# Performance work log

Measured on AMD Instinct MI355X. Metric: run time of the kernel, lower is better.

## Reference

```python
import jax, jax.numpy as jnp
import numpy as np

N, D = 16384, 2048


def setup_inputs() -> dict:
    key = jax.random.key(0)
    k1, k2, k3, k4 = jax.random.split(key, 4)
    X = jax.random.normal(k1, (N, D), dtype=jnp.float32)
    keep = jax.random.uniform(k4, (N, D)) > 0.5
    X = jnp.where(keep, X, 0.0)
    A = jax.random.normal(k2, (D, D), dtype=jnp.float32)
    b = jax.random.normal(k3, (D,), dtype=jnp.float32)
    return {"X": X, "A": A, "b": b}


def reference(X, A, b):
    # y_pred = X @ A.T + b
    y_pred = jnp.einsum('nd,kd->nk', X, A) + b  # [N, D]
    mask = X != 0
    masked = jnp.where(mask, y_pred, 0.0)
    row_sum = masked.sum(axis=1, keepdims=True)          # [N, 1]
    has_any = mask.any(axis=1, keepdims=True)            # [N, 1]
    y_out = jnp.where(mask, masked / row_sum, 0.0)
    # rows with an empty mask stay all-zero (matches the Python-loop guard)
    y_out = jnp.where(has_any, y_out, 0.0)
    return y_out
```

## Files before the change

### kernel.cpp

```cpp
#include <hip/hip_runtime.h>

#define N_ROWS 16384
#define D_DIM  2048
#define BM 128
#define BN 128
#define BK 32
#define NKT (D_DIM / BK)

typedef __attribute__((ext_vector_type(8)))  _Float16 half8;
typedef __attribute__((ext_vector_type(4)))  _Float16 half4_t;
typedef __attribute__((ext_vector_type(4)))  float floatx4;

typedef __attribute__((address_space(1))) const unsigned int as1_uint;
typedef __attribute__((address_space(3))) unsigned int as3_uint;

__device__ __forceinline__ void gload_lds16(const _Float16* g, _Float16* l) {
    __builtin_amdgcn_global_load_lds((as1_uint*)g, (as3_uint*)l, 16, 0, 0);
}

__global__ void split_all_kernel(const float4* __restrict__ Xs,
                                 half4_t* __restrict__ Xdh,
                                 half4_t* __restrict__ Xdl,
                                 unsigned char* __restrict__ mask,
                                 const float4* __restrict__ As,
                                 half4_t* __restrict__ Adh,
                                 half4_t* __restrict__ Adl,
                                 int nX8, int total8)
{
    int i = blockIdx.x * blockDim.x + threadIdx.x;
    if (i >= total8) return;

    const float4* src; half4_t* dh; half4_t* dl; int j; bool domask;
    if (i < nX8) { src = Xs; dh = Xdh; dl = Xdl; j = i;       domask = true;  }
    else         { src = As; dh = Adh; dl = Adl; j = i - nX8; domask = false; }

    float4 a = src[2 * j];
    float4 b = src[2 * j + 1];
    half4_t ha, la, hb, lb;
    ha[0] = (_Float16)a.x; ha[1] = (_Float16)a.y;
    ha[2] = (_Float16)a.z; ha[3] = (_Float16)a.w;
    la[0] = (_Float16)((a.x - (float)ha[0]) * 4096.0f);
    la[1] = (_Float16)((a.y - (float)ha[1]) * 4096.0f);
    la[2] = (_Float16)((a.z - (float)ha[2]) * 4096.0f);
    la[3] = (_Float16)((a.w - (float)ha[3]) * 4096.0f);
    hb[0] = (_Float16)b.x; hb[1] = (_Float16)b.y;
    hb[2] = (_Float16)b.z; hb[3] = (_Float16)b.w;
    lb[0] = (_Float16)((b.x - (float)hb[0]) * 4096.0f);
    lb[1] = (_Float16)((b.y - (float)hb[1]) * 4096.0f);
    lb[2] = (_Float16)((b.z - (float)hb[2]) * 4096.0f);
    lb[3] = (_Float16)((b.w - (float)hb[3]) * 4096.0f);
    dh[2 * j] = ha; dh[2 * j + 1] = hb;
    dl[2 * j] = la; dl[2 * j + 1] = lb;
    if (domask) {
        unsigned int m = 0;
        m |= (a.x != 0.0f) ? 0x01u : 0u;  m |= (a.y != 0.0f) ? 0x02u : 0u;
        m |= (a.z != 0.0f) ? 0x04u : 0u;  m |= (a.w != 0.0f) ? 0x08u : 0u;
        m |= (b.x != 0.0f) ? 0x10u : 0u;  m |= (b.y != 0.0f) ? 0x20u : 0u;
        m |= (b.z != 0.0f) ? 0x40u : 0u;  m |= (b.w != 0.0f) ? 0x80u : 0u;
        mask[j] = (unsigned char)m;
    }
}

__global__ __launch_bounds__(256, 2)
void gemm_presplit_kernel(const _Float16* __restrict__ Xh,
                          const _Float16* __restrict__ Xl,
                          const _Float16* __restrict__ Ah,
                          const _Float16* __restrict__ Al,
                          const unsigned char* __restrict__ maskbits,
                          const float* __restrict__ bias,
                          float* __restrict__ out,
                          float* __restrict__ partials)
{
    __shared__ __align__(16) _Float16 sXh[2][BM * BK];
    __shared__ __align__(16) _Float16 sXl[2][BM * BK];
    __shared__ __align__(16) _Float16 sAh[2][BN * BK];
    __shared__ __align__(16) _Float16 sAl[2][BN * BK];

    const int t   = threadIdx.x;
    const int bid = blockIdx.x;

    const int xcd    = bid & 7;
    const int local  = bid >> 3;
    const int r_tile = (xcd << 4) + (local & 15);
    const int c_tile = local >> 4;
    const int m0 = r_tile * BM;
    const int n0 = c_tile * BN;

    const int lane  = t & 63;
    const int w     = t >> 6;
    const int wr    = w >> 1;
    const int wc    = w & 1;
    const int lrow  = lane & 15;
    const int lslot = lane >> 4;

    floatx4 acc1[4][4], acc2[4][4];
    #pragma unroll
    for (int mi = 0; mi < 4; ++mi)
        #pragma unroll
        for (int ni = 0; ni < 4; ++ni)
            #pragma unroll
            for (int j = 0; j < 4; ++j) { acc1[mi][ni][j] = 0.f; acc2[mi][ni][j] = 0.f; }

    const _Float16* gsrc;
    _Float16* lb0; _Float16* lb1;
    if      (w == 0) { gsrc = Xh + (size_t)m0 * D_DIM; lb0 = &sXh[0][0]; lb1 = &sXh[1][0]; }
    else if (w == 1) { gsrc = Xl + (size_t)m0 * D_DIM; lb0 = &sXl[0][0]; lb1 = &sXl[1][0]; }
    else if (w == 2) { gsrc = Ah + (size_t)n0 * D_DIM; lb0 = &sAh[0][0]; lb1 = &sAh[1][0]; }
    else             { gsrc = Al + (size_t)n0 * D_DIM; lb0 = &sAl[0][0]; lb1 = &sAl[1][0]; }

    int off8[8];
    #pragma unroll
    for (int i = 0; i < 8; ++i) {
        int c = i * 64 + lane;
        int row = c >> 2;
        int sp  = c & 3;
        int kslot = sp ^ ((row >> 1) & 3);
        off8[i] = row * D_DIM + kslot * 8;
    }

    auto issue = [&](int buf, int kt) {
        _Float16* lb = buf ? lb1 : lb0;
        const _Float16* gk = gsrc + kt * BK;
        #pragma unroll
        for (int i = 0; i < 8; ++i)
            gload_lds16(gk + off8[i], lb + i * 512);
    };

    issue(0, 0);

    int cur = 0;
    for (int kt = 0; kt < NKT; ++kt) {
        __syncthreads();
        if (kt + 1 < NKT) issue(cur ^ 1, kt + 1);

        half8 bhf[4], blf[4];
        #pragma unroll
        for (int ni = 0; ni < 4; ++ni) {
            int row = wc * 64 + ni * 16 + lrow;
            int off = row * BK + ((lslot ^ ((row >> 1) & 3)) << 3);
            bhf[ni] = *reinterpret_cast<const half8*>(&sAh[cur][off]);
            blf[ni] = *reinterpret_cast<const half8*>(&sAl[cur][off]);
        }
        #pragma unroll
        for (int mi = 0; mi < 4; ++mi) {
            int row = wr * 64 + mi * 16 + lrow;
            int off = row * BK + ((lslot ^ ((row >> 1) & 3)) << 3);
            half8 ah = *reinterpret_cast<const half8*>(&sXh[cur][off]);
            half8 al = *reinterpret_cast<const half8*>(&sXl[cur][off]);
            #pragma unroll
            for (int ni = 0; ni < 4; ++ni) {
                acc1[mi][ni] = __builtin_amdgcn_mfma_f32_16x16x32_f16(ah, bhf[ni], acc1[mi][ni], 0, 0, 0);
                acc2[mi][ni] = __builtin_amdgcn_mfma_f32_16x16x32_f16(ah, blf[ni], acc2[mi][ni], 0, 0, 0);
                acc2[mi][ni] = __builtin_amdgcn_mfma_f32_16x16x32_f16(al, bhf[ni], acc2[mi][ni], 0, 0, 0);
            }
        }
        cur ^= 1;
    }

    #pragma unroll
    for (int mi = 0; mi < 4; ++mi) {
        float rs[4];
        #pragma unroll
        for (int j = 0; j < 4; ++j) rs[j] = 0.f;
        #pragma unroll
        for (int ni = 0; ni < 4; ++ni) {
            int c = n0 + wc * 64 + ni * 16 + lrow;
            float bv = bias[c];
            #pragma unroll
            for (int j = 0; j < 4; ++j) {
                int r = m0 + wr * 64 + mi * 16 + lslot * 4 + j;
                size_t idx = (size_t)r * D_DIM + c;
                float v = acc1[mi][ni][j] + acc2[mi][ni][j] * (1.0f / 4096.0f) + bv;
                unsigned int bit = (maskbits[idx >> 3] >> (c & 7)) & 1u;
                float mv = bit ? v : 0.0f;
                out[idx] = mv;
                rs[j] += mv;
            }
        }
        #pragma unroll
        for (int j = 0; j < 4; ++j) {
            float s = rs[j];
            s += __shfl_xor(s, 1, 64);
            s += __shfl_xor(s, 2, 64);
            s += __shfl_xor(s, 4, 64);
            s += __shfl_xor(s, 8, 64);
            if (lrow == 0) {
                int r = m0 + wr * 64 + mi * 16 + lslot * 4 + j;
                partials[(size_t)r * 32 + c_tile * 2 + wc] = s;
            }
        }
    }
}

__global__ void partial_inv_kernel(const float4* __restrict__ p4, float* __restrict__ inv)
{
    int gid  = blockIdx.x * 256 + threadIdx.x;
    int r    = gid >> 3;
    int slot = gid & 7;
    float4 v = p4[(size_t)r * 8 + slot];
    float s = (v.x + v.y) + (v.z + v.w);
    s += __shfl_xor(s, 1, 64);
    s += __shfl_xor(s, 2, 64);
    s += __shfl_xor(s, 4, 64);
    if (slot == 0) inv[r] = (s != 0.0f) ? (1.0f / s) : 0.0f;
}

__global__ __launch_bounds__(256, 2)
void gemm_mask_kernel(const float* __restrict__ X,
                      const float* __restrict__ A,
                      const float* __restrict__ bias,
                      float* __restrict__ out)
{
    __shared__ __align__(16) _Float16 sXh[2][BM * BK];
    __shared__ __align__(16) _Float16 sXl[2][BM * BK];
    __shared__ __align__(16) _Float16 sAh[2][BN * BK];
    __shared__ __align__(16) _Float16 sAl[2][BN * BK];

    const int t   = threadIdx.x;
    const int bid = blockIdx.x;
    const int xcd    = bid & 7;
    const int local  = bid >> 3;
    const int r_tile = (xcd << 4) + (local & 15);
    const int c_tile = local >> 4;
    const int m0 = r_tile * BM;
    const int n0 = c_tile * BN;

    const int lane  = t & 63;
    const int w     = t >> 6;
    const int wr    = w >> 1;
    const int wc    = w & 1;
    const int lrow  = lane & 15;
    const int lslot = lane >> 4;

    const float4* X4 = reinterpret_cast<const float4*>(X);
    const float4* A4 = reinterpret_cast<const float4*>(A);

    floatx4 acc1[4][4], acc2[4][4];
    #pragma unroll
    for (int mi = 0; mi < 4; ++mi)
        #pragma unroll
        for (int ni = 0; ni < 4; ++ni)
            #pragma unroll
            for (int j = 0; j < 4; ++j) { acc1[mi][ni][j] = 0.f; acc2[mi][ni][j] = 0.f; }

    float4 rx[4], ra[4];
    #pragma unroll
    for (int i = 0; i < 4; ++i) {
        int f = i * 256 + t; int row = f >> 3; int k4 = f & 7;
        rx[i] = X4[(size_t)(m0 + row) * (D_DIM / 4) + k4];
        ra[i] = A4[(size_t)(n0 + row) * (D_DIM / 4) + k4];
    }

    auto stage = [&](const float4* rv, _Float16* dsh, _Float16* dsl) {
        #pragma unroll
        for (int i = 0; i < 4; ++i) {
            int f = i * 256 + t; int row = f >> 3; int k4 = f & 7;
            float4 v = rv[i];
            half4_t h, l;
            h[0] = (_Float16)v.x; h[1] = (_Float16)v.y;
            h[2] = (_Float16)v.z; h[3] = (_Float16)v.w;
            l[0] = (_Float16)((v.x - (float)h[0]) * 4096.0f);
            l[1] = (_Float16)((v.y - (float)h[1]) * 4096.0f);
            l[2] = (_Float16)((v.z - (float)h[2]) * 4096.0f);
            l[3] = (_Float16)((v.w - (float)h[3]) * 4096.0f);
            int off = row * BK + ((((k4 >> 1) ^ ((row >> 1) & 3)) << 3) + ((k4 & 1) << 2));
            *reinterpret_cast<half4_t*>(dsh + off) = h;
            *reinterpret_cast<half4_t*>(dsl + off) = l;
        }
    };

    stage(rx, &sXh[0][0], &sXl[0][0]);
    stage(ra, &sAh[0][0], &sAl[0][0]);

    int cur = 0;
    for (int kt = 0; kt < NKT; ++kt) {
        __syncthreads();
        const bool more = (kt + 1 < NKT);
        if (more) {
            int kb = (kt + 1) * (BK / 4);
            #pragma unroll
            for (int i = 0; i < 4; ++i) {
                int f = i * 256 + t; int row = f >> 3; int k4 = f & 7;
                rx[i] = X4[(size_t)(m0 + row) * (D_DIM / 4) + kb + k4];
                ra[i] = A4[(size_t)(n0 + row) * (D_DIM / 4) + kb + k4];
            }
        }

        half8 bhf[4], blf[4];
        #pragma unroll
        for (int ni = 0; ni < 4; ++ni) {
            int row = wc * 64 + ni * 16 + lrow;
            int off = row * BK + ((lslot ^ ((row >> 1) & 3)) << 3);
            bhf[ni] = *reinterpret_cast<const half8*>(&sAh[cur][off]);
            blf[ni] = *reinterpret_cast<const half8*>(&sAl[cur][off]);
        }
        #pragma unroll
        for (int mi = 0; mi < 4; ++mi) {
            int row = wr * 64 + mi * 16 + lrow;
            int off = row * BK + ((lslot ^ ((row >> 1) & 3)) << 3);
            half8 ah = *reinterpret_cast<const half8*>(&sXh[cur][off]);
            half8 al = *reinterpret_cast<const half8*>(&sXl[cur][off]);
            #pragma unroll
            for (int ni = 0; ni < 4; ++ni) {
                acc1[mi][ni] = __builtin_amdgcn_mfma_f32_16x16x32_f16(ah, bhf[ni], acc1[mi][ni], 0, 0, 0);
                acc2[mi][ni] = __builtin_amdgcn_mfma_f32_16x16x32_f16(ah, blf[ni], acc2[mi][ni], 0, 0, 0);
                acc2[mi][ni] = __builtin_amdgcn_mfma_f32_16x16x32_f16(al, bhf[ni], acc2[mi][ni], 0, 0, 0);
            }
        }

        if (more) {
            int nxt = cur ^ 1;
            stage(rx, &sXh[nxt][0], &sXl[nxt][0]);
            stage(ra, &sAh[nxt][0], &sAl[nxt][0]);
            cur = nxt;
        }
    }

    #pragma unroll
    for (int mi = 0; mi < 4; ++mi) {
        #pragma unroll
        for (int ni = 0; ni < 4; ++ni) {
            int c = n0 + wc * 64 + ni * 16 + lrow;
            float bv = bias[c];
            #pragma unroll
            for (int j = 0; j < 4; ++j) {
                int r = m0 + wr * 64 + mi * 16 + lslot * 4 + j;
                float v = acc1[mi][ni][j] + acc2[mi][ni][j] * (1.0f / 4096.0f) + bv;
                float xv = X[(size_t)r * D_DIM + c];
                out[(size_t)r * D_DIM + c] = (xv != 0.0f) ? v : 0.0f;
            }
        }
    }
}

__global__ void row_sum_inv_kernel(const float* __restrict__ out, float* __restrict__ inv)
{
    int gw = (blockIdx.x * 256 + threadIdx.x) >> 6;
    int l  = threadIdx.x & 63;
    const float4* row = reinterpret_cast<const float4*>(out) + (size_t)gw * (D_DIM / 4);
    float s = 0.f;
    #pragma unroll
    for (int j = 0; j < 8; ++j) {
        float4 v = row[j * 64 + l];
        s += (v.x + v.y) + (v.z + v.w);
    }
    #pragma unroll
    for (int off = 32; off > 0; off >>= 1) s += __shfl_down(s, off, 64);
    if (l == 0) inv[gw] = (s != 0.0f) ? (1.0f / s) : 0.0f;
}

__global__ void scale_kernel(float* __restrict__ out, const float* __restrict__ inv)
{
    const int total = N_ROWS * (D_DIM / 4);
    float4* o = reinterpret_cast<float4*>(out);
    for (int i = blockIdx.x * blockDim.x + threadIdx.x; i < total;
         i += gridDim.x * blockDim.x) {
        float s  = inv[i >> 9];
        float4 v = o[i];
        v.x *= s; v.y *= s; v.z *= s; v.w *= s;
        o[i] = v;
    }
}

extern "C" void kernel_launch(void* const* d_in, const int* in_sizes, int n_in,
                              void* d_out, int out_size, void* d_ws, size_t ws_size,
                              hipStream_t stream)
{
    const float* X  = (const float*)d_in[0];
    const float* A  = (const float*)d_in[1];
    const float* b  = (const float*)d_in[2];
    float* out = (float*)d_out;

    const size_t nX = (size_t)N_ROWS * D_DIM;
    const size_t nA = (size_t)D_DIM * D_DIM;
    const size_t inv_bytes  = (size_t)N_ROWS * sizeof(float);
    const size_t part_bytes = (size_t)N_ROWS * 32 * sizeof(float);
    const size_t mask_bytes = nX / 8;
    const size_t need = inv_bytes + part_bytes + 2 * nX * 2 + 2 * nA * 2 + mask_bytes;

    if (ws_size >= need) {
        float*         inv  = (float*)d_ws;
        float*         part = (float*)((char*)d_ws + inv_bytes);
        _Float16*      Xh   = (_Float16*)((char*)d_ws + inv_bytes + part_bytes);
        _Float16*      Xl   = Xh + nX;
        _Float16*      Ah   = Xl + nX;
        _Float16*      Al   = Ah + nA;
        unsigned char* mb   = (unsigned char*)(Al + nA);

        const int nX8    = (int)(nX / 8);
        const int total8 = (int)((nX + nA) / 8);
        hipLaunchKernelGGL(split_all_kernel, dim3((total8 + 255) / 256), dim3(256), 0, stream,
                           (const float4*)X, (half4_t*)Xh, (half4_t*)Xl, mb,
                           (const float4*)A, (half4_t*)Ah, (half4_t*)Al,
                           nX8, total8);
        hipLaunchKernelGGL(gemm_presplit_kernel, dim3((N_ROWS / BM) * (D_DIM / BN)), dim3(256), 0, stream,
                           Xh, Xl, Ah, Al, mb, b, out, part);
        hipLaunchKernelGGL(partial_inv_kernel, dim3(N_ROWS * 8 / 256), dim3(256), 0, stream,
                           (const float4*)part, inv);
        hipLaunchKernelGGL(scale_kernel, dim3(2048), dim3(256), 0, stream, out, inv);
    } else {
        float* inv = (float*)d_ws;
        hipLaunchKernelGGL(gemm_mask_kernel, dim3((N_ROWS / BM) * (D_DIM / BN)), dim3(256), 0, stream,
                           X, A, b, out);
        hipLaunchKernelGGL(row_sum_inv_kernel, dim3(N_ROWS / 4), dim3(256), 0, stream, out, inv);
        hipLaunchKernelGGL(scale_kernel, dim3(2048), dim3(256), 0, stream, out, inv);
    }
}
```

Measured before the change: 479.0 us.

## Load A fragments directly from global and fuse row-sum inverse into scaling

The GEMM kernel stops staging the A operand (high and low halves) through LDS. Each wave now reads its B fragments straight from global memory every k-step, and all four waves share the X-tile async loads. This halves LDS usage and may allow higher occupancy, but it adds uncoalesced global or L2 reads of A with no software prefetch. Separately, the partial-sum-to-inverse kernel is merged into the scale kernel, saving one launch and the inv buffer round trip.

After: 714.1 us. 49.1% more time.

```diff
diff --git a/kernel.cpp b/kernel.cpp
--- a/kernel.cpp
+++ b/kernel.cpp
@@ -73,8 +73,6 @@
 {
     __shared__ __align__(16) _Float16 sXh[2][BM * BK];
     __shared__ __align__(16) _Float16 sXl[2][BM * BK];
-    __shared__ __align__(16) _Float16 sAh[2][BN * BK];
-    __shared__ __align__(16) _Float16 sAl[2][BN * BK];
 
     const int t   = threadIdx.x;
     const int bid = blockIdx.x;
@@ -101,32 +99,37 @@
             #pragma unroll
             for (int j = 0; j < 4; ++j) { acc1[mi][ni][j] = 0.f; acc2[mi][ni][j] = 0.f; }
 
-    const _Float16* gsrc;
-    _Float16* lb0; _Float16* lb1;
-    if      (w == 0) { gsrc = Xh + (size_t)m0 * D_DIM; lb0 = &sXh[0][0]; lb1 = &sXh[1][0]; }
-    else if (w == 1) { gsrc = Xl + (size_t)m0 * D_DIM; lb0 = &sXl[0][0]; lb1 = &sXl[1][0]; }
-    else if (w == 2) { gsrc = Ah + (size_t)n0 * D_DIM; lb0 = &sAh[0][0]; lb1 = &sAh[1][0]; }
-    else             { gsrc = Al + (size_t)n0 * D_DIM; lb0 = &sAl[0][0]; lb1 = &sAl[1][0]; }
-
-    int off8[8];
-    #pragma unroll
-    for (int i = 0; i < 8; ++i) {
-        int c = i * 64 + lane;
+    const _Float16* gsrc = (w < 2 ? Xh : Xl) + (size_t)m0 * D_DIM;
+    _Float16* lb0 = (w < 2) ? &sXh[0][0] : &sXl[0][0];
+    _Float16* lb1 = (w < 2) ? &sXh[1][0] : &sXl[1][0];
+    const int cbase = (w & 1) * 256;
+
+    int off4[8];
+    #pragma unroll
+    for (int i = 0; i < 4; ++i) {
+        int c = cbase + i * 64 + lane;
         int row = c >> 2;
         int sp  = c & 3;
         int kslot = sp ^ ((row >> 1) & 3);
-        off8[i] = row * D_DIM + kslot * 8;
+        off4[i] = row * D_DIM + kslot * 8;
     }
 
     auto issue = [&](int buf, int kt) {
-        _Float16* lb = buf ? lb1 : lb0;
+        _Float16* lb = (buf ? lb1 : lb0) + cbase * 8;
         const _Float16* gk = gsrc + kt * BK;
         #pragma unroll
-        for (int i = 0; i < 8; ++i)
-            gload_lds16(gk + off8[i], lb + i * 512);
+        for (int i = 0; i < 4; ++i)
+            gload_lds16(gk + off4[i], lb + i * 512);
     };
 
     issue(0, 0);
+
+    const _Float16* aH = Ah + (size_t)n0 * D_DIM;
+    const _Float16* aL = Al + (size_t)n0 * D_DIM;
+    int boff[4];
+    #pragma unroll
+    for (int ni = 0; ni < 4; ++ni)
+        boff[ni] = (wc * 64 + ni * 16 + lrow) * D_DIM + lslot * 8;
 
     int cur = 0;
     for (int kt = 0; kt < NKT; ++kt) {
@@ -136,10 +139,8 @@
         half8 bhf[4], blf[4];
         #pragma unroll
         for (int ni = 0; ni < 4; ++ni) {
-            int row = wc * 64 + ni * 16 + lrow;
-            int off = row * BK + ((lslot ^ ((row >> 1) & 3)) << 3);
-            bhf[ni] = *reinterpret_cast<const half8*>(&sAh[cur][off]);
-            blf[ni] = *reinterpret_cast<const half8*>(&sAl[cur][off]);
+            bhf[ni] = *reinterpret_cast<const half8*>(aH + boff[ni] + kt * BK);
+            blf[ni] = *reinterpret_cast<const half8*>(aL + boff[ni] + kt * BK);
         }
         #pragma unroll
         for (int mi = 0; mi < 4; ++mi) {
@@ -192,17 +193,25 @@
     }
 }
 
-__global__ void partial_inv_kernel(const float4* __restrict__ p4, float* __restrict__ inv)
-{
-    int gid  = blockIdx.x * 256 + threadIdx.x;
-    int r    = gid >> 3;
-    int slot = gid & 7;
-    float4 v = p4[(size_t)r * 8 + slot];
-    float s = (v.x + v.y) + (v.z + v.w);
-    s += __shfl_xor(s, 1, 64);
-    s += __shfl_xor(s, 2, 64);
-    s += __shfl_xor(s, 4, 64);
-    if (slot == 0) inv[r] = (s != 0.0f) ? (1.0f / s) : 0.0f;
+__global__ void scale_fused_kernel(float* __restrict__ out,
+                                   const float* __restrict__ partials)
+{
+    int r   = blockIdx.x * 8 + (threadIdx.x >> 5);
+    int l32 = threadIdx.x & 31;
+    float s = partials[(size_t)r * 32 + l32];
+    s += __shfl_xor(s, 1, 32);
+    s += __shfl_xor(s, 2, 32);
+    s += __shfl_xor(s, 4, 32);
+    s += __shfl_xor(s, 8, 32);
+    s += __shfl_xor(s, 16, 32);
+    float inv = (s != 0.0f) ? (1.0f / s) : 0.0f;
+    float4* rowp = reinterpret_cast<float4*>(out + (size_t)r * D_DIM);
+    #pragma unroll
+    for (int j = 0; j < 16; ++j) {
+        float4 v = rowp[j * 32 + l32];
+        v.x *= inv; v.y *= inv; v.z *= inv; v.w *= inv;
+        rowp[j * 32 + l32] = v;
+    }
 }
 
 __global__ __launch_bounds__(256, 2)
@@ -373,15 +382,13 @@
 
     const size_t nX = (size_t)N_ROWS * D_DIM;
     const size_t nA = (size_t)D_DIM * D_DIM;
-    const size_t inv_bytes  = (size_t)N_ROWS * sizeof(float);
     const size_t part_bytes = (size_t)N_ROWS * 32 * sizeof(float);
     const size_t mask_bytes = nX / 8;
-    const size_t need = inv_bytes + part_bytes + 2 * nX * 2 + 2 * nA * 2 + mask_bytes;
+    const size_t need = part_bytes + 2 * nX * 2 + 2 * nA * 2 + mask_bytes;
 
     if (ws_size >= need) {
-        float*         inv  = (float*)d_ws;
-        float*         part = (float*)((char*)d_ws + inv_bytes);
-        _Float16*      Xh   = (_Float16*)((char*)d_ws + inv_bytes + part_bytes);
+        float*         part = (float*)d_ws;
+        _Float16*      Xh   = (_Float16*)((char*)d_ws + part_bytes);
         _Float16*      Xl   = Xh + nX;
         _Float16*      Ah   = Xl + nX;
         _Float16*      Al   = Ah + nA;
@@ -395,9 +402,8 @@
                            nX8, total8);
         hipLaunchKernelGGL(gemm_presplit_kernel, dim3((N_ROWS / BM) * (D_DIM / BN)), dim3(256), 0, stream,
                            Xh, Xl, Ah, Al, mb, b, out, part);
-        hipLaunchKernelGGL(partial_inv_kernel, dim3(N_ROWS * 8 / 256), dim3(256), 0, stream,
-                           (const float4*)part, inv);
-        hipLaunchKernelGGL(scale_kernel, dim3(2048), dim3(256), 0, stream, out, inv);
+        hipLaunchKernelGGL(scale_fused_kernel, dim3(N_ROWS / 8), dim3(256), 0, stream,
+                           out, part);
     } else {
         float* inv = (float*)d_ws;
         hipLaunchKernelGGL(gemm_mask_kernel, dim3((N_ROWS / BM) * (D_DIM / BN)), dim3(256), 0, stream,
```
